# Performance work log

Measured on AMD Instinct MI355X. Metric: run time of the kernel, lower is better.

The kernel has to match this reference:

```python
import jax, jax.numpy as jnp
import numpy as np

NEG = -10000.0
START_TAG = 62
STOP_TAG = 63


def setup_inputs() -> dict:
    key = jax.random.key(0)
    k1, k2, k3 = jax.random.split(key, 3)
    S, B, T = 512, 512, 64
    feats = jax.random.normal(k1, (S, B, T), dtype=jnp.float32)
    tags = jax.random.randint(k2, (S, B), 0, START_TAG, dtype=jnp.int32)
    mask = jnp.ones((S, B), dtype=jnp.float32)
    # nn.Parameter(torch.randn(T,T)) with start row / stop col clamped to -1e4
    transitions = jax.random.normal(k3, (T, T), dtype=jnp.float32)
    transitions = transitions.at[START_TAG, :].set(NEG).at[:, STOP_TAG].set(NEG)
    return {"feats": feats, "tags": tags, "mask": mask, "transitions": transitions}


def _score_sentence(feats, tags, mask, transitions):
    # feats: [S,B,T], tags/mask: [S,B]
    S, B, T = feats.shape
    emission = jnp.take_along_axis(feats, tags[:, :, None], axis=2)[..., 0]  # [S,B]
    start = jnp.full((1, B), START_TAG, dtype=tags.dtype)
    tags_ext = jnp.concatenate([start, tags], axis=0)  # [S+1,B]
    trans = transitions[tags_ext[:-1], tags_ext[1:]]  # [S,B]
    score = jnp.sum((emission + trans) * mask, axis=0)  # [B]
    last_idx = mask.sum(axis=0).astype(jnp.int32) - 1  # [B]
    last_tags = tags[last_idx, jnp.arange(B)]
    return score + transitions[last_tags, STOP_TAG]


def _forward_alg(feats, mask, transitions):
    S, B, T = feats.shape
    log_alpha0 = jnp.full((B, T), NEG, dtype=feats.dtype).at[:, START_TAG].set(0.0)

    def step(log_alpha, xs):
        f_i, m_i = xs  # [B,T], [B]
        # broadcast: [B, prev_tag, next_tag]
        scores = log_alpha[:, :, None] + transitions[None, :, :] + f_i[:, None, :]
        nxt = jax.nn.logsumexp(scores, axis=1)  # [B,T]
        log_alpha = jnp.where(m_i[:, None] > 0, nxt, log_alpha)
        return log_alpha, None

    log_alpha, _ = jax.lax.scan(step, log_alpha0, (feats, mask))
    return jax.nn.logsumexp(log_alpha + transitions[STOP_TAG][None, :], axis=1)  # [B]


def reference(feats, tags, mask, transitions):
    score_true = _score_sentence(feats, tags, mask, transitions)
    log_z = _forward_alg(feats, mask, transitions)
    return jnp.mean(log_z - score_true)
```

## Files before the change

kernel.cpp:

```cpp
#include <hip/hip_runtime.h>

#define NEG (-10000.0f)
#define START_TAG 62
#define STOP_TAG 63
#define SLEN 512
#define BATCH 512
#define NTAG 64

__device__ __forceinline__ float readlane_f(float v, int lane) {
    return __uint_as_float(__builtin_amdgcn_readlane(__float_as_uint(v), lane));
}

__global__ __launch_bounds__(64) __attribute__((amdgpu_waves_per_eu(1, 1)))
void crf_fwd(const float* __restrict__ feats,
             const int* __restrict__ tags,
             const float* __restrict__ mask,
             const float* __restrict__ trans,
             float* __restrict__ diff ) {
    const int b = blockIdx.x;
    const int j = threadIdx.x;

    __shared__ float smask[SLEN];

    float e[NTAG];
    float colsum = 0.0f;
#pragma unroll
    for (int i = 0; i < NTAG; ++i) {
        e[i] = __expf(trans[i * NTAG + j]);
        colsum += e[i];
    }
    const float tstop = trans[STOP_TAG * NTAG + j];

    float mreg[8];
#pragma unroll
    for (int k = 0; k < 8; ++k) mreg[k] = mask[(64 * k + j) * BATCH + b];
#pragma unroll
    for (int k = 0; k < 8; ++k) smask[64 * k + j] = mreg[k];

    float f_s0 = feats[(size_t)b * NTAG + j];
    float m0 = readlane_f(mreg[0], 0);
    float alpha0 = (m0 > 0.0f) ? (NEG + log1pf(colsum) + f_s0)
                               : ((j == START_TAG) ? 0.0f : NEG);
    const float C0 = readlane_f(alpha0, START_TAG);
    float q = __expf(alpha0 - C0);

    if (j == 0) smask[0] = 0.0f;
    __syncthreads();

    const float* fp = feats + (size_t)b * NTAG + j;
    float fr[4];
#pragma unroll
    for (int t = 0; t < 4; ++t) fr[t] = fp[(size_t)t * BATCH * NTAG];

    float rinv = 1.0f;
    int kcur = 0;
    int ktot = 0;

    for (int blk = 0; blk < 128; ++blk) {
#pragma unroll
        for (int t = 0; t < 4; ++t) {
            const int s = blk * 4 + t;

            const float mk = smask[s];

            float ef = __expf(fr[t]);
            int sp = s + 4;
            if (sp > SLEN - 1) sp = SLEN - 1;
            fr[t] = fp[(size_t)sp * BATCH * NTAG];
            float efr = ef * rinv;

            unsigned qu = __float_as_uint(q);
            float su[64];
            float acc[4] = {0.0f, 0.0f, 0.0f, 0.0f};
#pragma unroll
            for (int i = 0; i < 8; ++i)
                su[i] = __uint_as_float(__builtin_amdgcn_readlane(qu, i));
#pragma unroll
            for (int i = 0; i < NTAG; ++i) {
                if (i < NTAG - 8)
                    su[i + 8] = __uint_as_float(
                        __builtin_amdgcn_readlane(qu, i + 8));
                acc[i & 3] = fmaf(su[i], e[i], acc[i & 3]);
            }
            float acc_s = (acc[0] + acc[1]) + (acc[2] + acc[3]);

            float qn = acc_s * efr;
            bool upd = (mk > 0.0f);
            q = upd ? qn : q;

            ktot = upd ? (ktot + kcur) : ktot;
            unsigned a0u = __builtin_amdgcn_readfirstlane(__float_as_uint(acc_s));
            int ke = (int)((a0u >> 23) & 0xffu) - 127;
            ke = (ke < -60) ? -60 : ((ke > 60) ? 60 : ke);
            float rnew = __uint_as_float((unsigned)(127 - ke) << 23);
            rinv = upd ? rnew : rinv;
            kcur = upd ? ke : kcur;
        }
    }

    float et = __expf(tstop);
    float pe = q * et;
#pragma unroll
    for (int w = 32; w >= 1; w >>= 1) pe += __shfl_xor(pe, w, 64);
    float logz = __logf(pe) + C0 + (float)ktot * 0.6931471805599453f;

    float psc = 0.0f, pms = 0.0f;
#pragma unroll
    for (int k = 0; k < 8; ++k) {
        int s = j + 64 * k;
        int tg = tags[s * BATCH + b];
        float mkk = mreg[k];
        int tprev = (s == 0) ? START_TAG : tags[(s - 1) * BATCH + b];
        float em = feats[((size_t)s * BATCH + b) * NTAG + tg];
        psc = fmaf(em + trans[tprev * NTAG + tg], mkk, psc);
        pms += mkk;
    }
#pragma unroll
    for (int w = 32; w >= 1; w >>= 1) {
        psc += __shfl_xor(psc, w, 64);
        pms += __shfl_xor(pms, w, 64);
    }

    if (j == 0) {
        int last_idx = (int)(pms + 0.5f) - 1;
        int ltag = tags[last_idx * BATCH + b];
        float score = psc + trans[ltag * NTAG + STOP_TAG];
        diff[b] = logz - score;
    }
}

__global__ __launch_bounds__(512) void crf_reduce(const float* __restrict__ diff,
                                                  float* __restrict__ out) {
    __shared__ float sdata[8];
    int t = threadIdx.x;
    float val = diff[t];
#pragma unroll
    for (int w = 32; w >= 1; w >>= 1)
        val += __shfl_xor(val, w, 64);
    if ((t & 63) == 0) sdata[t >> 6] = val;
    __syncthreads();
    if (t == 0) {
        float ssum = 0.0f;
        for (int i = 0; i < 8; ++i) ssum += sdata[i];
        out[0] = ssum * (1.0f / (float)BATCH);
    }
}

extern "C" void kernel_launch(void* const* d_in, const int* in_sizes, int n_in,
                              void* d_out, int out_size, void* d_ws, size_t ws_size,
                              hipStream_t stream) {
    const float* feats = (const float*)d_in[0];
    const int* tags = (const int*)d_in[1];
    const float* mask = (const float*)d_in[2];
    const float* trans = (const float*)d_in[3];
    float* out = (float*)d_out;
    float* diff = (float*)d_ws;

    crf_fwd<<<BATCH, 64, 0, stream>>>(feats, tags, mask, trans, diff);
    crf_reduce<<<1, 512, 0, stream>>>(diff, out);
}
```

Measured before the change: 232.9 us.

## Replace scalar readlane broadcast with XOR-permuted DPP/swizzle matvec exchange

The per-step 64x64 matvec previously broadcast each lane's q value through 64 readlane instructions into scalar registers. It now has each lane read its partners in XOR order, using quad-permute DPP moves, ds_swizzle for XOR masks inside 32 lanes, and one ds_bpermute for the half-wave swap. The transition exponentials are stored in the matching XOR-permuted order so each lane still accumulates the correct column. This trades serialized SALU readlanes for VALU DPP and LDS-crossbar swizzles, which carry their own latency on the serial recurrence.

```diff
diff --git a/kernel.cpp b/kernel.cpp
--- a/kernel.cpp
+++ b/kernel.cpp
@@ -11,6 +11,21 @@
     return __uint_as_float(__builtin_amdgcn_readlane(__float_as_uint(v), lane));
 }
 
+template <int XMASK>
+__device__ __forceinline__ float swz_xor(float v) {
+    return __uint_as_float(__builtin_amdgcn_ds_swizzle(
+        __float_as_uint(v), (XMASK << 10) | 0x1F));
+}
+
+template <int CTRL>
+__device__ __forceinline__ float dpp_qp(float v) {
+    return __uint_as_float(__builtin_amdgcn_mov_dpp(
+        __float_as_uint(v), CTRL, 0xF, 0xF, true));
+}
+#define QP_X1 0xB1
+#define QP_X2 0x4E
+#define QP_X3 0x1B
+
 __global__ __launch_bounds__(64) __attribute__((amdgpu_waves_per_eu(1, 1)))
 void crf_fwd(const float* __restrict__ feats,
              const int* __restrict__ tags,
@@ -22,12 +37,12 @@
 
     __shared__ float smask[SLEN];
 
-    float e[NTAG];
+    float ex[NTAG];
     float colsum = 0.0f;
 #pragma unroll
-    for (int i = 0; i < NTAG; ++i) {
-        e[i] = __expf(trans[i * NTAG + j]);
-        colsum += e[i];
+    for (int m = 0; m < NTAG; ++m) {
+        ex[m] = __expf(trans[((j ^ m) << 6) + j]);
+        colsum += ex[m];
     }
     const float tstop = trans[STOP_TAG * NTAG + j];
 
@@ -46,6 +61,8 @@
 
     if (j == 0) smask[0] = 0.0f;
     __syncthreads();
+
+    const int a32 = ((j ^ 32) << 2);
 
     const float* fp = feats + (size_t)b * NTAG + j;
     float fr[4];
@@ -69,20 +86,36 @@
             fr[t] = fp[(size_t)sp * BATCH * NTAG];
             float efr = ef * rinv;
 
-            unsigned qu = __float_as_uint(q);
-            float su[64];
-            float acc[4] = {0.0f, 0.0f, 0.0f, 0.0f};
-#pragma unroll
-            for (int i = 0; i < 8; ++i)
-                su[i] = __uint_as_float(__builtin_amdgcn_readlane(qu, i));
-#pragma unroll
-            for (int i = 0; i < NTAG; ++i) {
-                if (i < NTAG - 8)
-                    su[i + 8] = __uint_as_float(
-                        __builtin_amdgcn_readlane(qu, i + 8));
-                acc[i & 3] = fmaf(su[i], e[i], acc[i & 3]);
-            }
-            float acc_s = (acc[0] + acc[1]) + (acc[2] + acc[3]);
+            float q32 = __uint_as_float(__builtin_amdgcn_ds_bpermute(
+                a32, __float_as_uint(q)));
+
+            float acc0, acc1, acc2, acc3, qc;
+            acc0 = q * ex[0];
+            acc1 = dpp_qp<QP_X1>(q) * ex[1];
+            acc2 = dpp_qp<QP_X2>(q) * ex[2];
+            acc3 = dpp_qp<QP_X3>(q) * ex[3];
+#define GRP(QSRC, BASE)                                          \
+    acc0 = fmaf((QSRC), ex[(BASE) + 0], acc0);                   \
+    acc1 = fmaf(dpp_qp<QP_X1>(QSRC), ex[(BASE) + 1], acc1);      \
+    acc2 = fmaf(dpp_qp<QP_X2>(QSRC), ex[(BASE) + 2], acc2);      \
+    acc3 = fmaf(dpp_qp<QP_X3>(QSRC), ex[(BASE) + 3], acc3);
+            qc = swz_xor<4>(q);    GRP(qc, 4);
+            qc = swz_xor<8>(q);    GRP(qc, 8);
+            qc = swz_xor<12>(q);   GRP(qc, 12);
+            qc = swz_xor<16>(q);   GRP(qc, 16);
+            qc = swz_xor<20>(q);   GRP(qc, 20);
+            qc = swz_xor<24>(q);   GRP(qc, 24);
+            qc = swz_xor<28>(q);   GRP(qc, 28);
+            GRP(q32, 32);
+            qc = swz_xor<4>(q32);  GRP(qc, 36);
+            qc = swz_xor<8>(q32);  GRP(qc, 40);
+            qc = swz_xor<12>(q32); GRP(qc, 44);
+            qc = swz_xor<16>(q32); GRP(qc, 48);
+            qc = swz_xor<20>(q32); GRP(qc, 52);
+            qc = swz_xor<24>(q32); GRP(qc, 56);
+            qc = swz_xor<28>(q32); GRP(qc, 60);
+#undef GRP
+            float acc_s = (acc0 + acc1) + (acc2 + acc3);
 
             float qn = acc_s * efr;
             bool upd = (mk > 0.0f);
```

Measured after the change: 249.0 us. +6.9%, slower.

## Split tag recurrence across two waves with LDS exchange of partial sums

Applied to the files above, without the earlier changes.

Each block now uses two wavefronts. Each wave holds half of the exp-transition column and computes a partial dot product over 32 previous tags, reading the broadcast alpha vector from LDS as float4 loads instead of 64 scalar readlanes. The two partials are exchanged through a double-buffered LDS array with one block barrier per timestep. This shortens the serial per-step chain, at the cost of a barrier and LDS round trip every step and twice as many waves.

```diff
diff --git a/kernel.cpp b/kernel.cpp
--- a/kernel.cpp
+++ b/kernel.cpp
@@ -7,45 +7,64 @@
 #define BATCH 512
 #define NTAG 64
 
+typedef float f32x4 __attribute__((ext_vector_type(4)));
+
 __device__ __forceinline__ float readlane_f(float v, int lane) {
     return __uint_as_float(__builtin_amdgcn_readlane(__float_as_uint(v), lane));
 }
 
-__global__ __launch_bounds__(64) __attribute__((amdgpu_waves_per_eu(1, 1)))
+__global__ __launch_bounds__(128) __attribute__((amdgpu_waves_per_eu(1, 1)))
 void crf_fwd(const float* __restrict__ feats,
              const int* __restrict__ tags,
              const float* __restrict__ mask,
              const float* __restrict__ trans,
              float* __restrict__ diff ) {
     const int b = blockIdx.x;
-    const int j = threadIdx.x;
+    const int tid = threadIdx.x;
+    const int h = tid >> 6;
+    const int j = tid & 63;
 
-    __shared__ float smask[SLEN];
+    __shared__ float smask[SLEN + 1];
+    __shared__ __align__(16) float qbuf[NTAG];
+    __shared__ float pbuf[2][2][NTAG];
+    __shared__ float csum2[2][NTAG];
 
-    float e[NTAG];
-    float colsum = 0.0f;
+    float e[32];
+    float halfsum = 0.0f;
 #pragma unroll
-    for (int i = 0; i < NTAG; ++i) {
-        e[i] = __expf(trans[i * NTAG + j]);
-        colsum += e[i];
+    for (int ii = 0; ii < 32; ++ii) {
+        e[ii] = __expf(trans[(32 * h + ii) * NTAG + j]);
+        halfsum += e[ii];
     }
+    csum2[h][j] = halfsum;
     const float tstop = trans[STOP_TAG * NTAG + j];
 
-    float mreg[8];
 #pragma unroll
-    for (int k = 0; k < 8; ++k) mreg[k] = mask[(64 * k + j) * BATCH + b];
-#pragma unroll
-    for (int k = 0; k < 8; ++k) smask[64 * k + j] = mreg[k];
+    for (int k = 0; k < 4; ++k) {
+        int row = 64 * (4 * h + k) + j;
+        smask[row] = mask[row * BATCH + b];
+    }
+    if (tid == 0) { smask[SLEN] = 0.0f; }
+    __syncthreads();
+
+    const float colsum = csum2[0][j] + csum2[1][j];
 
     float f_s0 = feats[(size_t)b * NTAG + j];
-    float m0 = readlane_f(mreg[0], 0);
+    float m0 = mask[b];
     float alpha0 = (m0 > 0.0f) ? (NEG + log1pf(colsum) + f_s0)
                                : ((j == START_TAG) ? 0.0f : NEG);
     const float C0 = readlane_f(alpha0, START_TAG);
     float q = __expf(alpha0 - C0);
 
-    if (j == 0) smask[0] = 0.0f;
+    qbuf[j] = q;
+    if (tid == 0) smask[0] = 0.0f;
     __syncthreads();
+
+    const f32x4* qv = (const f32x4*)&qbuf[32 * h];
+    f32x4 Q[8];
+#pragma unroll
+    for (int c = 0; c < 8; ++c) Q[c] = qv[c];
+    float mk = smask[0];
 
     const float* fp = feats + (size_t)b * NTAG + j;
     float fr[4];
@@ -60,8 +79,7 @@
 #pragma unroll
         for (int t = 0; t < 4; ++t) {
             const int s = blk * 4 + t;
-
-            const float mk = smask[s];
+            const int ph = s & 1;
 
             float ef = __expf(fr[t]);
             int sp = s + 4;
@@ -69,24 +87,29 @@
             fr[t] = fp[(size_t)sp * BATCH * NTAG];
             float efr = ef * rinv;
 
-            unsigned qu = __float_as_uint(q);
-            float su[64];
-            float acc[4] = {0.0f, 0.0f, 0.0f, 0.0f};
+            float a0 = 0.0f, a1 = 0.0f, a2 = 0.0f, a3 = 0.0f;
 #pragma unroll
-            for (int i = 0; i < 8; ++i)
-                su[i] = __uint_as_float(__builtin_amdgcn_readlane(qu, i));
-#pragma unroll
-            for (int i = 0; i < NTAG; ++i) {
-                if (i < NTAG - 8)
-                    su[i + 8] = __uint_as_float(
-                        __builtin_amdgcn_readlane(qu, i + 8));
-                acc[i & 3] = fmaf(su[i], e[i], acc[i & 3]);
+            for (int c = 0; c < 8; ++c) {
+                a0 = fmaf(Q[c].x, e[4 * c + 0], a0);
+                a1 = fmaf(Q[c].y, e[4 * c + 1], a1);
+                a2 = fmaf(Q[c].z, e[4 * c + 2], a2);
+                a3 = fmaf(Q[c].w, e[4 * c + 3], a3);
             }
-            float acc_s = (acc[0] + acc[1]) + (acc[2] + acc[3]);
+            float p = (a0 + a1) + (a2 + a3);
+
+            pbuf[ph][h][j] = p;
+            __syncthreads();
+            float po = pbuf[ph][1 - h][j];
+            float acc_s = p + po;
 
             float qn = acc_s * efr;
             bool upd = (mk > 0.0f);
             q = upd ? qn : q;
+
+            qbuf[j] = q;
+#pragma unroll
+            for (int c = 0; c < 8; ++c) Q[c] = qv[c];
+            mk = smask[s + 1];
 
             ktot = upd ? (ktot + kcur) : ktot;
             unsigned a0u = __builtin_amdgcn_readfirstlane(__float_as_uint(acc_s));
@@ -97,6 +120,8 @@
             kcur = upd ? ke : kcur;
         }
     }
+
+    if (h != 0) return;
 
     float et = __expf(tstop);
     float pe = q * et;
@@ -109,7 +134,7 @@
     for (int k = 0; k < 8; ++k) {
         int s = j + 64 * k;
         int tg = tags[s * BATCH + b];
-        float mkk = mreg[k];
+        float mkk = mask[(64 * k + j) * BATCH + b];
         int tprev = (s == 0) ? START_TAG : tags[(s - 1) * BATCH + b];
         float em = feats[((size_t)s * BATCH + b) * NTAG + tg];
         psc = fmaf(em + trans[tprev * NTAG + tg], mkk, psc);
@@ -121,7 +146,7 @@
         pms += __shfl_xor(pms, w, 64);
     }
 
-    if (j == 0) {
+    if (tid == 0) {
         int last_idx = (int)(pms + 0.5f) - 1;
         int ltag = tags[last_idx * BATCH + b];
         float score = psc + trans[ltag * NTAG + STOP_TAG];
@@ -156,6 +181,6 @@
     float* out = (float*)d_out;
     float* diff = (float*)d_ws;
 
-    crf_fwd<<<BATCH, 64, 0, stream>>>(feats, tags, mask, trans, diff);
+    crf_fwd<<<BATCH, 128, 0, stream>>>(feats, tags, mask, trans, diff);
     crf_reduce<<<1, 512, 0, stream>>>(diff, out);
 }
```

After: 235.5 us. About the same (+1.1%).
